# Optimization experiments

Hardware: AMD Instinct MI355X
Metric: run time of the kernel (lower is better)

Reference implementation:

```python
import jax, jax.numpy as jnp
import numpy as np

B, T, D = 32, 1024, 1024  # batch, t_k (encoder steps), attn_sz == cell_state_sz


def setup_inputs() -> dict:
    key = jax.random.key(0)
    ks = jax.random.split(key, 7)
    scale = 1.0 / np.sqrt(D)
    return {
        "h_i": jax.random.normal(ks[0], (B, T, D), jnp.float32),
        "s_t": jax.random.normal(ks[1], (B, D), jnp.float32),
        "coverage": jax.random.uniform(ks[2], (B, T), jnp.float32),
        "W_h": jax.random.normal(ks[3], (D, D), jnp.float32) * scale,
        "W_s": jax.random.normal(ks[4], (D, D), jnp.float32) * scale,
        "b_s": jnp.zeros((D,), jnp.float32),
        "W_c": jax.random.normal(ks[5], (D,), jnp.float32) * scale,  # Dense(1 -> D) kernel
        "V_w": jax.random.normal(ks[6], (D,), jnp.float32) * scale,  # Dense(D -> 1) kernel
    }


def reference(h_i, s_t, coverage, W_h, W_s, b_s, W_c, V_w):
    # enc_features = W_h(h_i): (B, T, D)
    enc_features = jnp.einsum("btd,de->bte", h_i, W_h)
    # dec_features = W_s(s_t) broadcast over time: (B, 1, D)
    dec_features = (s_t @ W_s + b_s)[:, None, :]
    # coverage features: scalar coverage per step times (1->D) kernel
    cov_features = coverage[:, :, None] * W_c[None, None, :]
    features = enc_features + dec_features + cov_features
    # e_t = V(tanh(features)) squeezed to (B, T)
    e_t = jnp.einsum("btd,d->bt", jnp.tanh(features), V_w)
    a_t = jax.nn.softmax(e_t, axis=1)
    coverage_new = coverage + a_t
    # context = a_t @ h_i : (B, D)
    context_vector = jnp.einsum("bt,btd->bd", a_t, h_i)
    return context_vector, a_t, coverage_new
```

## Files before the change

kernel.cpp:

```cpp
#include <hip/hip_runtime.h>

#define B_ 32
#define T_ 1024
#define D_ 1024
#define M_ (B_ * T_)
#define NT_ 8
#define BM_ 128
#define BN_ 128
#define BK_ 64
#define NKT (D_ / BK_)
#define LSTR 72

#define FENCE_ALL() asm volatile("s_waitcnt vmcnt(0) lgkmcnt(0)" ::: "memory")

typedef __attribute__((ext_vector_type(8))) short short8;
typedef __attribute__((ext_vector_type(4))) float f32x4;

__device__ __forceinline__ unsigned f2bf(float f) {
    union { float f; unsigned u; } v; v.f = f;
    return (v.u + 0x7FFFu + ((v.u >> 16) & 1u)) >> 16;
}
__device__ __forceinline__ unsigned pack2(float a, float b) {
    return f2bf(a) | (f2bf(b) << 16);
}
__device__ __forceinline__ float bf2f(unsigned hi16) {
    union { unsigned u; float f; } v; v.u = hi16 << 16;
    return v.f;
}
__device__ __forceinline__ float fast_tanh(float x) {
    x = fminf(15.0f, fmaxf(-15.0f, x));
    float e = __expf(2.0f * x);
    return (e - 1.0f) * __fdividef(1.0f, e + 1.0f);
}

__global__ __launch_bounds__(256) void conv_h_kernel(
    const float* __restrict__ in, uint4* __restrict__ out)
{
    const int idx = blockIdx.x * 256 + threadIdx.x;
    const int stride = gridDim.x * 256;
    const int ngroups = M_ * D_ / 8;
    const float4* in4 = (const float4*)in;
    for (int g = idx; g < ngroups; g += stride) {
        const float4 a = in4[2 * g];
        const float4 b = in4[2 * g + 1];
        out[g] = make_uint4(pack2(a.x, a.y), pack2(a.z, a.w),
                            pack2(b.x, b.y), pack2(b.z, b.w));
    }
}

__global__ __launch_bounds__(256) void conv_wt_kernel(
    const float* __restrict__ W_h, unsigned short* __restrict__ Wt)
{
    __shared__ float tile[64][65];
    const int k0 = (blockIdx.x & 15) * 64;
    const int n0 = (blockIdx.x >> 4) * 64;
    const int tx = threadIdx.x & 63, ty = threadIdx.x >> 6;
#pragma unroll
    for (int r = 0; r < 16; ++r) {
        const int row = ty * 16 + r;
        tile[row][tx] = W_h[(size_t)(k0 + row) * D_ + n0 + tx];
    }
    __syncthreads();
#pragma unroll
    for (int r = 0; r < 16; ++r) {
        const int row = ty * 16 + r;
        Wt[(size_t)(n0 + row) * D_ + k0 + tx] = (unsigned short)f2bf(tile[tx][row]);
    }
}

__global__ __launch_bounds__(256) void dec_kernel(
    const float* __restrict__ s_t, const float* __restrict__ W_s,
    const float* __restrict__ b_s, float* __restrict__ dec_part)
{
    const int bid = blockIdx.x;
    const int kc = bid & 3;
    const int nc = (bid >> 2) & 3;
    const int b  = bid >> 4;
    const int d = nc * 256 + threadIdx.x;
    const int k0 = kc * 256;
    __shared__ float s_lds[256];
    s_lds[threadIdx.x] = s_t[b * D_ + k0 + threadIdx.x];
    __syncthreads();
    float acc = (kc == 0) ? b_s[d] : 0.f;
#pragma unroll 8
    for (int k = 0; k < 256; ++k) acc += s_lds[k] * W_s[(size_t)(k0 + k) * D_ + d];
    dec_part[kc * (B_ * D_) + b * D_ + d] = acc;
}

__global__ __launch_bounds__(256, 2) void attn_gemm_fast(
    const unsigned short* __restrict__ h_bf, const unsigned short* __restrict__ wt_bf,
    const float* __restrict__ dec_part, const float* __restrict__ coverage,
    const float* __restrict__ W_c, const float* __restrict__ V_w,
    float* __restrict__ e_part)
{
    __shared__ __align__(16) unsigned short lA[BM_ * BK_];
    __shared__ __align__(16) unsigned short lB[BN_ * BK_];
    __shared__ float e_red[256];

    const int tid = threadIdx.x;
    const int nt = blockIdx.x >> 8;
    const int mt = blockIdx.x & 255;
    const int m0 = mt * BM_;
    const int n0 = nt * BN_;
    const int bb = m0 >> 10;

    const int wave = tid >> 6;
    const int lane = tid & 63;
    const int wr = wave >> 1, wc = wave & 1;
    const int lr = lane & 15;
    const int lk = lane >> 4;

    f32x4 acc[4][4];
    const f32x4 fzero = {0.f, 0.f, 0.f, 0.f};
#pragma unroll
    for (int i = 0; i < 4; ++i)
#pragma unroll
        for (int j = 0; j < 4; ++j) acc[i][j] = fzero;

    const char* gA = (const char*)h_bf + (size_t)m0 * (D_ * 2);
    const char* gB = (const char*)wt_bf + (size_t)n0 * (D_ * 2);
    const int lrow8 = lane >> 3;
    const int scol = (((lane & 7) ^ lrow8) << 4);

    for (int k0 = 0; k0 < D_; k0 += BK_) {
#pragma unroll
        for (int j = 0; j < 4; ++j) {
            const int c = 4 * wave + j;
            const int row = c * 8 + lrow8;
            const size_t goff = (size_t)row * (D_ * 2) + (size_t)k0 * 2 + scol;
            __builtin_amdgcn_global_load_lds(
                (const __attribute__((address_space(1))) void*)(gA + goff),
                (__attribute__((address_space(3))) void*)((char*)lA + c * 1024),
                16, 0, 0);
            __builtin_amdgcn_global_load_lds(
                (const __attribute__((address_space(1))) void*)(gB + goff),
                (__attribute__((address_space(3))) void*)((char*)lB + c * 1024),
                16, 0, 0);
        }
        FENCE_ALL();
        __syncthreads();

        short8 af[2][4], bfr[2][4];
        const int sw = (lr & 7) << 4;
#pragma unroll
        for (int kk = 0; kk < 2; ++kk)
#pragma unroll
            for (int i = 0; i < 4; ++i) {
                const int ar = wr * 64 + i * 16 + lr;
                const int br = wc * 64 + i * 16 + lr;
                const int kb = kk * 64 + lk * 16;
                af[kk][i]  = *(const short8*)((const char*)lA + ar * 128 + (kb ^ sw));
                bfr[kk][i] = *(const short8*)((const char*)lB + br * 128 + (kb ^ sw));
            }
#pragma unroll
        for (int kk = 0; kk < 2; ++kk)
#pragma unroll
            for (int mi = 0; mi < 4; ++mi)
#pragma unroll
                for (int ni = 0; ni < 4; ++ni)
                    acc[mi][ni] = __builtin_amdgcn_mfma_f32_16x16x32_bf16(
                        af[kk][mi], bfr[kk][ni], acc[mi][ni], 0, 0, 0);
        FENCE_ALL();
        __syncthreads();
    }

    float esum[4][4];
    float covv[4][4];
#pragma unroll
    for (int mi = 0; mi < 4; ++mi)
#pragma unroll
        for (int r = 0; r < 4; ++r) {
            esum[mi][r] = 0.f;
            covv[mi][r] = coverage[m0 + wr * 64 + mi * 16 + lk * 4 + r];
        }
    const float* dp = dec_part + bb * D_;
#pragma unroll
    for (int ni = 0; ni < 4; ++ni) {
        const int n = n0 + wc * 64 + ni * 16 + lr;
        const float vw = V_w[n];
        const float dc = dp[n] + dp[B_ * D_ + n] + dp[2 * B_ * D_ + n] + dp[3 * B_ * D_ + n];
        const float wcv = W_c[n];
#pragma unroll
        for (int mi = 0; mi < 4; ++mi)
#pragma unroll
            for (int r = 0; r < 4; ++r) {
                const float f = acc[mi][ni][r] + dc + covv[mi][r] * wcv;
                esum[mi][r] += fast_tanh(f) * vw;
            }
    }
#pragma unroll
    for (int off = 1; off <= 8; off <<= 1)
#pragma unroll
        for (int mi = 0; mi < 4; ++mi)
#pragma unroll
            for (int r = 0; r < 4; ++r)
                esum[mi][r] += __shfl_xor(esum[mi][r], off, 64);

    if (lr == 0) {
#pragma unroll
        for (int mi = 0; mi < 4; ++mi)
#pragma unroll
            for (int r = 0; r < 4; ++r)
                e_red[wc * 128 + wr * 64 + mi * 16 + lk * 4 + r] = esum[mi][r];
    }
    FENCE_ALL();
    __syncthreads();
    if (tid < 128)
        e_part[(size_t)nt * M_ + m0 + tid] = e_red[tid] + e_red[128 + tid];
}

__global__ __launch_bounds__(256, 2) void attn_gemm_kernel(
    const float* __restrict__ h_i, const float* __restrict__ W_h,
    const float* __restrict__ dec_part, const float* __restrict__ coverage,
    const float* __restrict__ W_c, const float* __restrict__ V_w,
    float* __restrict__ e_part)
{
    __shared__ __align__(16) unsigned short lA[BM_][LSTR];
    __shared__ __align__(16) unsigned short lB[BN_][LSTR];
    __shared__ float e_red[256];

    const int tid = threadIdx.x;
    const int nt = blockIdx.x >> 8;
    const int mt = blockIdx.x & 255;
    const int m0 = mt * BM_;
    const int n0 = nt * BN_;
    const int bb = m0 >> 10;

    const int wave = tid >> 6;
    const int lane = tid & 63;
    const int wr = wave >> 1, wc = wave & 1;
    const int lr = lane & 15;
    const int lk = lane >> 4;

    f32x4 acc[4][4];
    const f32x4 fzero = {0.f, 0.f, 0.f, 0.f};
#pragma unroll
    for (int i = 0; i < 4; ++i)
#pragma unroll
        for (int j = 0; j < 4; ++j) acc[i][j] = fzero;

    const int a_row = tid >> 4;
    const int a_k = (tid & 15) << 2;
    const float* hA = h_i + (size_t)m0 * D_;

    for (int k0 = 0; k0 < D_; k0 += BK_) {
#pragma unroll
        for (int p = 0; p < 8; ++p) {
            const int row = a_row + p * 16;
            const float4 v = *(const float4*)(hA + (size_t)row * D_ + (k0 + a_k));
            *(uint2*)&lA[row][a_k] = make_uint2(pack2(v.x, v.y), pack2(v.z, v.w));
        }
#pragma unroll
        for (int p = 0; p < 8; ++p) {
            const int task = tid + p * 256;
            const int n = task & 127;
            const int kg = task >> 7;
            const float* wp = W_h + (size_t)(k0 + kg * 4) * D_ + n0 + n;
            const float x0 = wp[0 * D_], x1 = wp[1 * D_], x2 = wp[2 * D_], x3 = wp[3 * D_];
            *(uint2*)&lB[n][kg * 4] = make_uint2(pack2(x0, x1), pack2(x2, x3));
        }
        __syncthreads();

        short8 af[2][4], bfr[2][4];
#pragma unroll
        for (int kk = 0; kk < 2; ++kk)
#pragma unroll
            for (int i = 0; i < 4; ++i) {
                af[kk][i]  = *(const short8*)&lA[wr * 64 + i * 16 + lr][kk * 32 + lk * 8];
                bfr[kk][i] = *(const short8*)&lB[wc * 64 + i * 16 + lr][kk * 32 + lk * 8];
            }
#pragma unroll
        for (int kk = 0; kk < 2; ++kk)
#pragma unroll
            for (int mi = 0; mi < 4; ++mi)
#pragma unroll
                for (int ni = 0; ni < 4; ++ni)
                    acc[mi][ni] = __builtin_amdgcn_mfma_f32_16x16x32_bf16(
                        af[kk][mi], bfr[kk][ni], acc[mi][ni], 0, 0, 0);
        __syncthreads();
    }

    float esum[4][4];
    float covv[4][4];
#pragma unroll
    for (int mi = 0; mi < 4; ++mi)
#pragma unroll
        for (int r = 0; r < 4; ++r) {
            esum[mi][r] = 0.f;
            covv[mi][r] = coverage[m0 + wr * 64 + mi * 16 + lk * 4 + r];
        }
    const float* dp = dec_part + bb * D_;
#pragma unroll
    for (int ni = 0; ni < 4; ++ni) {
        const int n = n0 + wc * 64 + ni * 16 + lr;
        const float vw = V_w[n];
        const float dc = dp[n] + dp[B_ * D_ + n] + dp[2 * B_ * D_ + n] + dp[3 * B_ * D_ + n];
        const float wcv = W_c[n];
#pragma unroll
        for (int mi = 0; mi < 4; ++mi)
#pragma unroll
            for (int r = 0; r < 4; ++r) {
                const float f = acc[mi][ni][r] + dc + covv[mi][r] * wcv;
                esum[mi][r] += fast_tanh(f) * vw;
            }
    }
#pragma unroll
    for (int off = 1; off <= 8; off <<= 1)
#pragma unroll
        for (int mi = 0; mi < 4; ++mi)
#pragma unroll
            for (int r = 0; r < 4; ++r)
                esum[mi][r] += __shfl_xor(esum[mi][r], off, 64);

    if (lr == 0) {
#pragma unroll
        for (int mi = 0; mi < 4; ++mi)
#pragma unroll
            for (int r = 0; r < 4; ++r)
                e_red[wc * 128 + wr * 64 + mi * 16 + lk * 4 + r] = esum[mi][r];
    }
    __syncthreads();
    if (tid < 128)
        e_part[(size_t)nt * M_ + m0 + tid] = e_red[tid] + e_red[128 + tid];
}

__global__ __launch_bounds__(256) void softmax_kernel(
    const float* __restrict__ e_part, const float* __restrict__ coverage,
    float* __restrict__ a_out, float* __restrict__ cov_out,
    float* __restrict__ a_ws)
{
    const int b = blockIdx.x;
    const int tid = threadIdx.x;
    __shared__ float redmx[4], redsum[4];
    float e[4];
#pragma unroll
    for (int j = 0; j < 4; ++j) {
        const int t = tid + j * 256;
        float s = 0.f;
#pragma unroll
        for (int p = 0; p < NT_; ++p) s += e_part[(size_t)p * M_ + b * T_ + t];
        e[j] = s;
    }
    float mx = fmaxf(fmaxf(e[0], e[1]), fmaxf(e[2], e[3]));
#pragma unroll
    for (int off = 32; off > 0; off >>= 1) mx = fmaxf(mx, __shfl_xor(mx, off, 64));
    if ((tid & 63) == 0) redmx[tid >> 6] = mx;
    __syncthreads();
    mx = fmaxf(fmaxf(redmx[0], redmx[1]), fmaxf(redmx[2], redmx[3]));
    float p4[4];
    float ps = 0.f;
#pragma unroll
    for (int j = 0; j < 4; ++j) { p4[j] = __expf(e[j] - mx); ps += p4[j]; }
#pragma unroll
    for (int off = 32; off > 0; off >>= 1) ps += __shfl_xor(ps, off, 64);
    if ((tid & 63) == 0) redsum[tid >> 6] = ps;
    __syncthreads();
    ps = redsum[0] + redsum[1] + redsum[2] + redsum[3];
    const float inv = __fdividef(1.f, ps);
#pragma unroll
    for (int j = 0; j < 4; ++j) {
        const int idx = b * T_ + tid + j * 256;
        const float a = p4[j] * inv;
        a_out[idx] = a;
        a_ws[idx] = a;
        cov_out[idx] = coverage[idx] + a;
    }
}

__global__ __launch_bounds__(256) void ctx_part_bf(
    const unsigned short* __restrict__ h_bf, const float* __restrict__ a_t,
    float* __restrict__ ctx_part)
{
    const int bid = blockIdx.x;
    const int b = bid >> 3;
    const int dc = (bid >> 2) & 1;
    const int tc = bid & 3;
    const int tid = threadIdx.x;
    const int d0 = dc * 512 + tid * 2;
    __shared__ float a_lds[256];
    a_lds[tid] = a_t[b * T_ + tc * 256 + tid];
    __syncthreads();
    const unsigned short* hp = h_bf + ((size_t)(b * T_ + tc * 256)) * D_ + d0;
    float acc0 = 0.f, acc1 = 0.f;
#pragma unroll 8
    for (int t = 0; t < 256; ++t) {
        const unsigned v = *(const unsigned*)(hp + (size_t)t * D_);
        const float a = a_lds[t];
        acc0 += a * bf2f(v & 0xFFFFu);
        acc1 += a * bf2f(v >> 16);
    }
    *(float2*)(ctx_part + tc * (B_ * D_) + b * D_ + d0) = make_float2(acc0, acc1);
}

__global__ __launch_bounds__(256) void ctx_part_f32(
    const float* __restrict__ h_i, const float* __restrict__ a_t,
    float* __restrict__ ctx_part)
{
    const int bid = blockIdx.x;
    const int b = bid >> 4;
    const int dc = (bid >> 2) & 3;
    const int tc = bid & 3;
    const int tid = threadIdx.x;
    const int d = dc * 256 + tid;
    __shared__ float a_lds[256];
    a_lds[tid] = a_t[b * T_ + tc * 256 + tid];
    __syncthreads();
    const float* hp = h_i + ((size_t)(b * T_ + tc * 256)) * D_ + d;
    float acc = 0.f;
#pragma unroll 8
    for (int t = 0; t < 256; ++t) acc += a_lds[t] * hp[(size_t)t * D_];
    ctx_part[tc * (B_ * D_) + b * D_ + d] = acc;
}

__global__ __launch_bounds__(256) void ctx_reduce_kernel(
    const float* __restrict__ ctx_part, float* __restrict__ out)
{
    const int i = blockIdx.x * 256 + threadIdx.x;
    out[i] = ctx_part[i] + ctx_part[B_ * D_ + i] + ctx_part[2 * B_ * D_ + i] +
             ctx_part[3 * B_ * D_ + i];
}

extern "C" void kernel_launch(void* const* d_in, const int* in_sizes, int n_in,
                              void* d_out, int out_size, void* d_ws, size_t ws_size,
                              hipStream_t stream)
{
    (void)in_sizes; (void)n_in; (void)out_size;
    const float* h_i      = (const float*)d_in[0];
    const float* s_t      = (const float*)d_in[1];
    const float* coverage = (const float*)d_in[2];
    const float* W_h      = (const float*)d_in[3];
    const float* W_s      = (const float*)d_in[4];
    const float* b_s      = (const float*)d_in[5];
    const float* W_c      = (const float*)d_in[6];
    const float* V_w      = (const float*)d_in[7];

    float* out     = (float*)d_out;
    float* ctx_out = out;
    float* a_out   = out + B_ * T_;
    float* cov_out = out + 2 * B_ * T_;

    float* ws       = (float*)d_ws;
    float* dec_part = ws;
    float* e_part   = dec_part + 4 * B_ * D_;
    float* ctx_part = e_part + NT_ * M_;
    float* a_ws     = ctx_part + 4 * B_ * D_;
    const size_t f32_count = 8 * (size_t)B_ * D_ + (size_t)NT_ * M_ + (size_t)B_ * T_;
    unsigned short* h_bf  = (unsigned short*)(ws + f32_count);
    unsigned short* wt_bf = h_bf + (size_t)M_ * D_;
    const size_t need = f32_count * 4 + ((size_t)M_ * D_ + (size_t)D_ * D_) * 2;

    dec_kernel<<<B_ * 16, 256, 0, stream>>>(s_t, W_s, b_s, dec_part);
    if (ws_size >= need) {
        conv_h_kernel<<<2048, 256, 0, stream>>>(h_i, (uint4*)h_bf);
        conv_wt_kernel<<<256, 256, 0, stream>>>(W_h, wt_bf);
        attn_gemm_fast<<<NT_ * (M_ / BM_), 256, 0, stream>>>(h_bf, wt_bf, dec_part,
                                                             coverage, W_c, V_w, e_part);
        softmax_kernel<<<B_, 256, 0, stream>>>(e_part, coverage, a_out, cov_out, a_ws);
        ctx_part_bf<<<B_ * 8, 256, 0, stream>>>(h_bf, a_ws, ctx_part);
    } else {
        attn_gemm_kernel<<<NT_ * (M_ / BM_), 256, 0, stream>>>(h_i, W_h, dec_part,
                                                               coverage, W_c, V_w, e_part);
        softmax_kernel<<<B_, 256, 0, stream>>>(e_part, coverage, a_out, cov_out, a_ws);
        ctx_part_f32<<<B_ * 16, 256, 0, stream>>>(h_i, a_ws, ctx_part);
    }
    ctx_reduce_kernel<<<(B_ * D_) / 256, 256, 0, stream>>>(ctx_part, ctx_out);
}
```

Measured before the change: 157.3 us.

## Fuse prep kernels, reorder GEMM tile mapping, prefetch next K tile in GEMM

Merges the h/W_h bf16 conversion kernels and the decoder projection into one prep launch, cutting two launches and letting the three run concurrently. In attn_gemm_fast, block indices now map with N-tiles innermost, so the 8 blocks sharing one h row tile are adjacent, which should improve L2 reuse of A. The K loop now issues the global-to-LDS loads for the next tile right after reading fragments, so they overlap with the MFMAs. This needs an extra barrier per iteration and uses a single LDS buffer, so overlap is limited to the MFMA phase.

```diff
diff --git a/kernel.cpp b/kernel.cpp
--- a/kernel.cpp
+++ b/kernel.cpp
@@ -33,39 +33,396 @@
     return (e - 1.0f) * __fdividef(1.0f, e + 1.0f);
 }
 
-__global__ __launch_bounds__(256) void conv_h_kernel(
-    const float* __restrict__ in, uint4* __restrict__ out)
-{
-    const int idx = blockIdx.x * 256 + threadIdx.x;
-    const int stride = gridDim.x * 256;
-    const int ngroups = M_ * D_ / 8;
-    const float4* in4 = (const float4*)in;
-    for (int g = idx; g < ngroups; g += stride) {
-        const float4 a = in4[2 * g];
-        const float4 b = in4[2 * g + 1];
-        out[g] = make_uint4(pack2(a.x, a.y), pack2(a.z, a.w),
-                            pack2(b.x, b.y), pack2(b.z, b.w));
-    }
-}
-
-__global__ __launch_bounds__(256) void conv_wt_kernel(
-    const float* __restrict__ W_h, unsigned short* __restrict__ Wt)
-{
-    __shared__ float tile[64][65];
-    const int k0 = (blockIdx.x & 15) * 64;
-    const int n0 = (blockIdx.x >> 4) * 64;
-    const int tx = threadIdx.x & 63, ty = threadIdx.x >> 6;
-#pragma unroll
-    for (int r = 0; r < 16; ++r) {
-        const int row = ty * 16 + r;
-        tile[row][tx] = W_h[(size_t)(k0 + row) * D_ + n0 + tx];
-    }
-    __syncthreads();
-#pragma unroll
-    for (int r = 0; r < 16; ++r) {
-        const int row = ty * 16 + r;
-        Wt[(size_t)(n0 + row) * D_ + k0 + tx] = (unsigned short)f2bf(tile[tx][row]);
-    }
+#define PREP_CONVH_BLKS 2048
+#define PREP_CONVWT_BLKS 256
+#define PREP_DEC_BLKS (B_ * 16)
+__global__ __launch_bounds__(256) void prep_kernel(
+    const float* __restrict__ h_i, uint4* __restrict__ h_bf4,
+    const float* __restrict__ W_h, unsigned short* __restrict__ Wt,
+    const float* __restrict__ s_t, const float* __restrict__ W_s,
+    const float* __restrict__ b_s, float* __restrict__ dec_part)
+{
+    __shared__ float smem[64 * 65];
+    const int bid = blockIdx.x;
+    const int tid = threadIdx.x;
+    if (bid < PREP_CONVH_BLKS) {
+        const int idx = bid * 256 + tid;
+        const int stride = PREP_CONVH_BLKS * 256;
+        const int ngroups = M_ * D_ / 8;
+        const float4* in4 = (const float4*)h_i;
+        for (int g = idx; g < ngroups; g += stride) {
+            const float4 a = in4[2 * g];
+            const float4 b = in4[2 * g + 1];
+            h_bf4[g] = make_uint4(pack2(a.x, a.y), pack2(a.z, a.w),
+                                  pack2(b.x, b.y), pack2(b.z, b.w));
+        }
+    } else if (bid < PREP_CONVH_BLKS + PREP_CONVWT_BLKS) {
+        const int tb = bid - PREP_CONVH_BLKS;
+        float (*tile)[65] = (float (*)[65])smem;
+        const int k0 = (tb & 15) * 64;
+        const int n0 = (tb >> 4) * 64;
+        const int tx = tid & 63, ty = tid >> 6;
+#pragma unroll
+        for (int r = 0; r < 16; ++r) {
+            const int row = ty * 16 + r;
+            tile[row][tx] = W_h[(size_t)(k0 + row) * D_ + n0 + tx];
+        }
+        __syncthreads();
+#pragma unroll
+        for (int r = 0; r < 16; ++r) {
+            const int row = ty * 16 + r;
+            Wt[(size_t)(n0 + row) * D_ + k0 + tx] = (unsigned short)f2bf(tile[tx][row]);
+        }
+    } else {
+        const int db = bid - (PREP_CONVH_BLKS + PREP_CONVWT_BLKS);
+        const int kc = db & 3;
+        const int nc = (db >> 2) & 3;
+        const int b  = db >> 4;
+        const int d = nc * 256 + tid;
+        const int k0 = kc * 256;
+        float* s_lds = smem;
+        s_lds[tid] = s_t[b * D_ + k0 + tid];
+        __syncthreads();
+        float acc = (kc == 0) ? b_s[d] : 0.f;
+#pragma unroll 8
+        for (int k = 0; k < 256; ++k) acc += s_lds[k] * W_s[(size_t)(k0 + k) * D_ + d];
+        dec_part[kc * (B_ * D_) + b * D_ + d] = acc;
+    }
+}
+
+__global__ __launch_bounds__(256, 2) void attn_gemm_fast(
+    const unsigned short* __restrict__ h_bf, const unsigned short* __restrict__ wt_bf,
+    const float* __restrict__ dec_part, const float* __restrict__ coverage,
+    const float* __restrict__ W_c, const float* __restrict__ V_w,
+    float* __restrict__ e_part)
+{
+    __shared__ __align__(16) unsigned short lA[BM_ * BK_];
+    __shared__ __align__(16) unsigned short lB[BN_ * BK_];
+    __shared__ float e_red[256];
+
+    const int tid = threadIdx.x;
+    const int mt = blockIdx.x >> 3;
+    const int nt = blockIdx.x & 7;
+    const int m0 = mt * BM_;
+    const int n0 = nt * BN_;
+    const int bb = m0 >> 10;
+
+    const int wave = tid >> 6;
+    const int lane = tid & 63;
+    const int wr = wave >> 1, wc = wave & 1;
+    const int lr = lane & 15;
+    const int lk = lane >> 4;
+
+    f32x4 acc[4][4];
+    const f32x4 fzero = {0.f, 0.f, 0.f, 0.f};
+#pragma unroll
+    for (int i = 0; i < 4; ++i)
+#pragma unroll
+        for (int j = 0; j < 4; ++j) acc[i][j] = fzero;
+
+    const char* gA = (const char*)h_bf + (size_t)m0 * (D_ * 2);
+    const char* gB = (const char*)wt_bf + (size_t)n0 * (D_ * 2);
+    const int lrow8 = lane >> 3;
+    const int scol = (((lane & 7) ^ lrow8) << 4);
+
+#define STAGE(k0)                                                                  \
+    {                                                                              \
+        _Pragma("unroll")                                                          \
+        for (int j = 0; j < 4; ++j) {                                              \
+            const int c = 4 * wave + j;                                            \
+            const int row = c * 8 + lrow8;                                         \
+            const size_t goff = (size_t)row * (D_ * 2) + (size_t)(k0) * 2 + scol;  \
+            __builtin_amdgcn_global_load_lds(                                      \
+                (const __attribute__((address_space(1))) void*)(gA + goff),        \
+                (__attribute__((address_space(3))) void*)((char*)lA + c * 1024),   \
+                16, 0, 0);                                                         \
+            __builtin_amdgcn_global_load_lds(                                      \
+                (const __attribute__((address_space(1))) void*)(gB + goff),        \
+                (__attribute__((address_space(3))) void*)((char*)lB + c * 1024),   \
+                16, 0, 0);                                                         \
+        }                                                                          \
+    }
+
+    STAGE(0);
+    const int sw = (lr & 7) << 4;
+
+    for (int kt = 0; kt < NKT; ++kt) {
+        FENCE_ALL();
+        __syncthreads();
+
+        short8 af[2][4], bfr[2][4];
+#pragma unroll
+        for (int kk = 0; kk < 2; ++kk)
+#pragma unroll
+            for (int i = 0; i < 4; ++i) {
+                const int ar = wr * 64 + i * 16 + lr;
+                const int br = wc * 64 + i * 16 + lr;
+                const int kb = kk * 64 + lk * 16;
+                af[kk][i]  = *(const short8*)((const char*)lA + ar * 128 + (kb ^ sw));
+                bfr[kk][i] = *(const short8*)((const char*)lB + br * 128 + (kb ^ sw));
+            }
+        FENCE_ALL();
+        __syncthreads();
+
+        if (kt + 1 < NKT) STAGE((kt + 1) * BK_);
+
+#pragma unroll
+        for (int kk = 0; kk < 2; ++kk)
+#pragma unroll
+            for (int mi = 0; mi < 4; ++mi)
+#pragma unroll
+                for (int ni = 0; ni < 4; ++ni)
+                    acc[mi][ni] = __builtin_amdgcn_mfma_f32_16x16x32_bf16(
+                        af[kk][mi], bfr[kk][ni], acc[mi][ni], 0, 0, 0);
+    }
+#undef STAGE
+
+    float esum[4][4];
+    float covv[4][4];
+#pragma unroll
+    for (int mi = 0; mi < 4; ++mi)
+#pragma unroll
+        for (int r = 0; r < 4; ++r) {
+            esum[mi][r] = 0.f;
+            covv[mi][r] = coverage[m0 + wr * 64 + mi * 16 + lk * 4 + r];
+        }
+    const float* dp = dec_part + bb * D_;
+#pragma unroll
+    for (int ni = 0; ni < 4; ++ni) {
+        const int n = n0 + wc * 64 + ni * 16 + lr;
+        const float vw = V_w[n];
+        const float dc = dp[n] + dp[B_ * D_ + n] + dp[2 * B_ * D_ + n] + dp[3 * B_ * D_ + n];
+        const float wcv = W_c[n];
+#pragma unroll
+        for (int mi = 0; mi < 4; ++mi)
+#pragma unroll
+            for (int r = 0; r < 4; ++r) {
+                const float f = acc[mi][ni][r] + dc + covv[mi][r] * wcv;
+                esum[mi][r] += fast_tanh(f) * vw;
+            }
+    }
+#pragma unroll
+    for (int off = 1; off <= 8; off <<= 1)
+#pragma unroll
+        for (int mi = 0; mi < 4; ++mi)
+#pragma unroll
+            for (int r = 0; r < 4; ++r)
+                esum[mi][r] += __shfl_xor(esum[mi][r], off, 64);
+
+    if (lr == 0) {
+#pragma unroll
+        for (int mi = 0; mi < 4; ++mi)
+#pragma unroll
+            for (int r = 0; r < 4; ++r)
+                e_red[wc * 128 + wr * 64 + mi * 16 + lk * 4 + r] = esum[mi][r];
+    }
+    FENCE_ALL();
+    __syncthreads();
+    if (tid < 128)
+        e_part[(size_t)nt * M_ + m0 + tid] = e_red[tid] + e_red[128 + tid];
+}
+
+__global__ __launch_bounds__(256, 2) void attn_gemm_kernel(
+    const float* __restrict__ h_i, const float* __restrict__ W_h,
+    const float* __restrict__ dec_part, const float* __restrict__ coverage,
+    const float* __restrict__ W_c, const float* __restrict__ V_w,
+    float* __restrict__ e_part)
+{
+    __shared__ __align__(16) unsigned short lA[BM_][LSTR];
+    __shared__ __align__(16) unsigned short lB[BN_][LSTR];
+    __shared__ float e_red[256];
+
+    const int tid = threadIdx.x;
+    const int nt = blockIdx.x >> 8;
+    const int mt = blockIdx.x & 255;
+    const int m0 = mt * BM_;
+    const int n0 = nt * BN_;
+    const int bb = m0 >> 10;
+
+    const int wave = tid >> 6;
+    const int lane = tid & 63;
+    const int wr = wave >> 1, wc = wave & 1;
+    const int lr = lane & 15;
+    const int lk = lane >> 4;
+
+    f32x4 acc[4][4];
+    const f32x4 fzero = {0.f, 0.f, 0.f, 0.f};
+#pragma unroll
+    for (int i = 0; i < 4; ++i)
+#pragma unroll
+        for (int j = 0; j < 4; ++j) acc[i][j] = fzero;
+
+    const int a_row = tid >> 4;
+    const int a_k = (tid & 15) << 2;
+    const float* hA = h_i + (size_t)m0 * D_;
+
+    for (int k0 = 0; k0 < D_; k0 += BK_) {
+#pragma unroll
+        for (int p = 0; p < 8; ++p) {
+            const int row = a_row + p * 16;
+            const float4 v = *(const float4*)(hA + (size_t)row * D_ + (k0 + a_k));
+            *(uint2*)&lA[row][a_k] = make_uint2(pack2(v.x, v.y), pack2(v.z, v.w));
+        }
+#pragma unroll
+        for (int p = 0; p < 8; ++p) {
+            const int task = tid + p * 256;
+            const int n = task & 127;
+            const int kg = task >> 7;
+            const float* wp = W_h + (size_t)(k0 + kg * 4) * D_ + n0 + n;
+            const float x0 = wp[0 * D_], x1 = wp[1 * D_], x2 = wp[2 * D_], x3 = wp[3 * D_];
+            *(uint2*)&lB[n][kg * 4] = make_uint2(pack2(x0, x1), pack2(x2, x3));
+        }
+        __syncthreads();
+
+        short8 af[2][4], bfr[2][4];
+#pragma unroll
+        for (int kk = 0; kk < 2; ++kk)
+#pragma unroll
+            for (int i = 0; i < 4; ++i) {
+                af[kk][i]  = *(const short8*)&lA[wr * 64 + i * 16 + lr][kk * 32 + lk * 8];
+                bfr[kk][i] = *(const short8*)&lB[wc * 64 + i * 16 + lr][kk * 32 + lk * 8];
+            }
+#pragma unroll
+        for (int kk = 0; kk < 2; ++kk)
+#pragma unroll
+            for (int mi = 0; mi < 4; ++mi)
+#pragma unroll
+                for (int ni = 0; ni < 4; ++ni)
+                    acc[mi][ni] = __builtin_amdgcn_mfma_f32_16x16x32_bf16(
+                        af[kk][mi], bfr[kk][ni], acc[mi][ni], 0, 0, 0);
+        __syncthreads();
+    }
+
+    float esum[4][4];
+    float covv[4][4];
+#pragma unroll
+    for (int mi = 0; mi < 4; ++mi)
+#pragma unroll
+        for (int r = 0; r < 4; ++r) {
+            esum[mi][r] = 0.f;
+            covv[mi][r] = coverage[m0 + wr * 64 + mi * 16 + lk * 4 + r];
+        }
+    const float* dp = dec_part + bb * D_;
+#pragma unroll
+    for (int ni = 0; ni < 4; ++ni) {
+        const int n = n0 + wc * 64 + ni * 16 + lr;
+        const float vw = V_w[n];
+        const float dc = dp[n] + dp[B_ * D_ + n] + dp[2 * B_ * D_ + n] + dp[3 * B_ * D_ + n];
+        const float wcv = W_c[n];
+#pragma unroll
+        for (int mi = 0; mi < 4; ++mi)
+#pragma unroll
+            for (int r = 0; r < 4; ++r) {
+                const float f = acc[mi][ni][r] + dc + covv[mi][r] * wcv;
+                esum[mi][r] += fast_tanh(f) * vw;
+            }
+    }
+#pragma unroll
+    for (int off = 1; off <= 8; off <<= 1)
+#pragma unroll
+        for (int mi = 0; mi < 4; ++mi)
+#pragma unroll
+            for (int r = 0; r < 4; ++r)
+                esum[mi][r] += __shfl_xor(esum[mi][r], off, 64);
+
+    if (lr == 0) {
+#pragma unroll
+        for (int mi = 0; mi < 4; ++mi)
+#pragma unroll
+            for (int r = 0; r < 4; ++r)
+                e_red[wc * 128 + wr * 64 + mi * 16 + lk * 4 + r] = esum[mi][r];
+    }
+    __syncthreads();
+    if (tid < 128)
+        e_part[(size_t)nt * M_ + m0 + tid] = e_red[tid] + e_red[128 + tid];
+}
+
+__global__ __launch_bounds__(256) void softmax_kernel(
+    const float* __restrict__ e_part, const float* __restrict__ coverage,
+    float* __restrict__ a_out, float* __restrict__ cov_out,
+    float* __restrict__ a_ws)
+{
+    const int b = blockIdx.x;
+    const int tid = threadIdx.x;
+    __shared__ float redmx[4], redsum[4];
+    float e[4];
+#pragma unroll
+    for (int j = 0; j < 4; ++j) {
+        const int t = tid + j * 256;
+        float s = 0.f;
+#pragma unroll
+        for (int p = 0; p < NT_; ++p) s += e_part[(size_t)p * M_ + b * T_ + t];
+        e[j] = s;
+    }
+    float mx = fmaxf(fmaxf(e[0], e[1]), fmaxf(e[2], e[3]));
+#pragma unroll
+    for (int off = 32; off > 0; off >>= 1) mx = fmaxf(mx, __shfl_xor(mx, off, 64));
+    if ((tid & 63) == 0) redmx[tid >> 6] = mx;
+    __syncthreads();
+    mx = fmaxf(fmaxf(redmx[0], redmx[1]), fmaxf(redmx[2], redmx[3]));
+    float p4[4];
+    float ps = 0.f;
+#pragma unroll
+    for (int j = 0; j < 4; ++j) { p4[j] = __expf(e[j] - mx); ps += p4[j]; }
+#pragma unroll
+    for (int off = 32; off > 0; off >>= 1) ps += __shfl_xor(ps, off, 64);
+    if ((tid & 63) == 0) redsum[tid >> 6] = ps;
+    __syncthreads();
+    ps = redsum[0] + redsum[1] + redsum[2] + redsum[3];
+    const float inv = __fdividef(1.f, ps);
+#pragma unroll
+    for (int j = 0; j < 4; ++j) {
+        const int idx = b * T_ + tid + j * 256;
+        const float a = p4[j] * inv;
+        a_out[idx] = a;
+        a_ws[idx] = a;
+        cov_out[idx] = coverage[idx] + a;
+    }
+}
+
+__global__ __launch_bounds__(256) void ctx_part_bf(
+    const unsigned short* __restrict__ h_bf, const float* __restrict__ a_t,
+    float* __restrict__ ctx_part)
+{
+    const int bid = blockIdx.x;
+    const int b = bid >> 3;
+    const int dc = (bid >> 2) & 1;
+    const int tc = bid & 3;
+    const int tid = threadIdx.x;
+    const int d0 = dc * 512 + tid * 2;
+    __shared__ float a_lds[256];
+    a_lds[tid] = a_t[b * T_ + tc * 256 + tid];
+    __syncthreads();
+    const unsigned short* hp = h_bf + ((size_t)(b * T_ + tc * 256)) * D_ + d0;
+    float acc0 = 0.f, acc1 = 0.f;
+#pragma unroll 8
+    for (int t = 0; t < 256; ++t) {
+        const unsigned v = *(const unsigned*)(hp + (size_t)t * D_);
+        const float a = a_lds[t];
+        acc0 += a * bf2f(v & 0xFFFFu);
+        acc1 += a * bf2f(v >> 16);
+    }
+    *(float2*)(ctx_part + tc * (B_ * D_) + b * D_ + d0) = make_float2(acc0, acc1);
+}
+
+__global__ __launch_bounds__(256) void ctx_part_f32(
+    const float* __restrict__ h_i, const float* __restrict__ a_t,
+    float* __restrict__ ctx_part)
+{
+    const int bid = blockIdx.x;
+    const int b = bid >> 4;
+    const int dc = (bid >> 2) & 3;
+    const int tc = bid & 3;
+    const int tid = threadIdx.x;
+    const int d = dc * 256 + tid;
+    __shared__ float a_lds[256];
+    a_lds[tid] = a_t[b * T_ + tc * 256 + tid];
+    __syncthreads();
+    const float* hp = h_i + ((size_t)(b * T_ + tc * 256)) * D_ + d;
+    float acc = 0.f;
+#pragma unroll 8
+    for (int t = 0; t < 256; ++t) acc += a_lds[t] * hp[(size_t)t * D_];
+    ctx_part[tc * (B_ * D_) + b * D_ + d] = acc;
 }
 
 __global__ __launch_bounds__(256) void dec_kernel(
@@ -85,331 +442,6 @@
 #pragma unroll 8
     for (int k = 0; k < 256; ++k) acc += s_lds[k] * W_s[(size_t)(k0 + k) * D_ + d];
     dec_part[kc * (B_ * D_) + b * D_ + d] = acc;
-}
-
-__global__ __launch_bounds__(256, 2) void attn_gemm_fast(
-    const unsigned short* __restrict__ h_bf, const unsigned short* __restrict__ wt_bf,
-    const float* __restrict__ dec_part, const float* __restrict__ coverage,
-    const float* __restrict__ W_c, const float* __restrict__ V_w,
-    float* __restrict__ e_part)
-{
-    __shared__ __align__(16) unsigned short lA[BM_ * BK_];
-    __shared__ __align__(16) unsigned short lB[BN_ * BK_];
-    __shared__ float e_red[256];
-
-    const int tid = threadIdx.x;
-    const int nt = blockIdx.x >> 8;
-    const int mt = blockIdx.x & 255;
-    const int m0 = mt * BM_;
-    const int n0 = nt * BN_;
-    const int bb = m0 >> 10;
-
-    const int wave = tid >> 6;
-    const int lane = tid & 63;
-    const int wr = wave >> 1, wc = wave & 1;
-    const int lr = lane & 15;
-    const int lk = lane >> 4;
-
-    f32x4 acc[4][4];
-    const f32x4 fzero = {0.f, 0.f, 0.f, 0.f};
-#pragma unroll
-    for (int i = 0; i < 4; ++i)
-#pragma unroll
-        for (int j = 0; j < 4; ++j) acc[i][j] = fzero;
-
-    const char* gA = (const char*)h_bf + (size_t)m0 * (D_ * 2);
-    const char* gB = (const char*)wt_bf + (size_t)n0 * (D_ * 2);
-    const int lrow8 = lane >> 3;
-    const int scol = (((lane & 7) ^ lrow8) << 4);
-
-    for (int k0 = 0; k0 < D_; k0 += BK_) {
-#pragma unroll
-        for (int j = 0; j < 4; ++j) {
-            const int c = 4 * wave + j;
-            const int row = c * 8 + lrow8;
-            const size_t goff = (size_t)row * (D_ * 2) + (size_t)k0 * 2 + scol;
-            __builtin_amdgcn_global_load_lds(
-                (const __attribute__((address_space(1))) void*)(gA + goff),
-                (__attribute__((address_space(3))) void*)((char*)lA + c * 1024),
-                16, 0, 0);
-            __builtin_amdgcn_global_load_lds(
-                (const __attribute__((address_space(1))) void*)(gB + goff),
-                (__attribute__((address_space(3))) void*)((char*)lB + c * 1024),
-                16, 0, 0);
-        }
-        FENCE_ALL();
-        __syncthreads();
-
-        short8 af[2][4], bfr[2][4];
-        const int sw = (lr & 7) << 4;
-#pragma unroll
-        for (int kk = 0; kk < 2; ++kk)
-#pragma unroll
-            for (int i = 0; i < 4; ++i) {
-                const int ar = wr * 64 + i * 16 + lr;
-                const int br = wc * 64 + i * 16 + lr;
-                const int kb = kk * 64 + lk * 16;
-                af[kk][i]  = *(const short8*)((const char*)lA + ar * 128 + (kb ^ sw));
-                bfr[kk][i] = *(const short8*)((const char*)lB + br * 128 + (kb ^ sw));
-            }
-#pragma unroll
-        for (int kk = 0; kk < 2; ++kk)
-#pragma unroll
-            for (int mi = 0; mi < 4; ++mi)
-#pragma unroll
-                for (int ni = 0; ni < 4; ++ni)
-                    acc[mi][ni] = __builtin_amdgcn_mfma_f32_16x16x32_bf16(
-                        af[kk][mi], bfr[kk][ni], acc[mi][ni], 0, 0, 0);
-        FENCE_ALL();
-        __syncthreads();
-    }
-
-    float esum[4][4];
-    float covv[4][4];
-#pragma unroll
-    for (int mi = 0; mi < 4; ++mi)
-#pragma unroll
-        for (int r = 0; r < 4; ++r) {
-            esum[mi][r] = 0.f;
-            covv[mi][r] = coverage[m0 + wr * 64 + mi * 16 + lk * 4 + r];
-        }
-    const float* dp = dec_part + bb * D_;
-#pragma unroll
-    for (int ni = 0; ni < 4; ++ni) {
-        const int n = n0 + wc * 64 + ni * 16 + lr;
-        const float vw = V_w[n];
-        const float dc = dp[n] + dp[B_ * D_ + n] + dp[2 * B_ * D_ + n] + dp[3 * B_ * D_ + n];
-        const float wcv = W_c[n];
-#pragma unroll
-        for (int mi = 0; mi < 4; ++mi)
-#pragma unroll
-            for (int r = 0; r < 4; ++r) {
-                const float f = acc[mi][ni][r] + dc + covv[mi][r] * wcv;
-                esum[mi][r] += fast_tanh(f) * vw;
-            }
-    }
-#pragma unroll
-    for (int off = 1; off <= 8; off <<= 1)
-#pragma unroll
-        for (int mi = 0; mi < 4; ++mi)
-#pragma unroll
-            for (int r = 0; r < 4; ++r)
-                esum[mi][r] += __shfl_xor(esum[mi][r], off, 64);
-
-    if (lr == 0) {
-#pragma unroll
-        for (int mi = 0; mi < 4; ++mi)
-#pragma unroll
-            for (int r = 0; r < 4; ++r)
-                e_red[wc * 128 + wr * 64 + mi * 16 + lk * 4 + r] = esum[mi][r];
-    }
-    FENCE_ALL();
-    __syncthreads();
-    if (tid < 128)
-        e_part[(size_t)nt * M_ + m0 + tid] = e_red[tid] + e_red[128 + tid];
-}
-
-__global__ __launch_bounds__(256, 2) void attn_gemm_kernel(
-    const float* __restrict__ h_i, const float* __restrict__ W_h,
-    const float* __restrict__ dec_part, const float* __restrict__ coverage,
-    const float* __restrict__ W_c, const float* __restrict__ V_w,
-    float* __restrict__ e_part)
-{
-    __shared__ __align__(16) unsigned short lA[BM_][LSTR];
-    __shared__ __align__(16) unsigned short lB[BN_][LSTR];
-    __shared__ float e_red[256];
-
-    const int tid = threadIdx.x;
-    const int nt = blockIdx.x >> 8;
-    const int mt = blockIdx.x & 255;
-    const int m0 = mt * BM_;
-    const int n0 = nt * BN_;
-    const int bb = m0 >> 10;
-
-    const int wave = tid >> 6;
-    const int lane = tid & 63;
-    const int wr = wave >> 1, wc = wave & 1;
-    const int lr = lane & 15;
-    const int lk = lane >> 4;
-
-    f32x4 acc[4][4];
-    const f32x4 fzero = {0.f, 0.f, 0.f, 0.f};
-#pragma unroll
-    for (int i = 0; i < 4; ++i)
-#pragma unroll
-        for (int j = 0; j < 4; ++j) acc[i][j] = fzero;
-
-    const int a_row = tid >> 4;
-    const int a_k = (tid & 15) << 2;
-    const float* hA = h_i + (size_t)m0 * D_;
-
-    for (int k0 = 0; k0 < D_; k0 += BK_) {
-#pragma unroll
-        for (int p = 0; p < 8; ++p) {
-            const int row = a_row + p * 16;
-            const float4 v = *(const float4*)(hA + (size_t)row * D_ + (k0 + a_k));
-            *(uint2*)&lA[row][a_k] = make_uint2(pack2(v.x, v.y), pack2(v.z, v.w));
-        }
-#pragma unroll
-        for (int p = 0; p < 8; ++p) {
-            const int task = tid + p * 256;
-            const int n = task & 127;
-            const int kg = task >> 7;
-            const float* wp = W_h + (size_t)(k0 + kg * 4) * D_ + n0 + n;
-            const float x0 = wp[0 * D_], x1 = wp[1 * D_], x2 = wp[2 * D_], x3 = wp[3 * D_];
-            *(uint2*)&lB[n][kg * 4] = make_uint2(pack2(x0, x1), pack2(x2, x3));
-        }
-        __syncthreads();
-
-        short8 af[2][4], bfr[2][4];
-#pragma unroll
-        for (int kk = 0; kk < 2; ++kk)
-#pragma unroll
-            for (int i = 0; i < 4; ++i) {
-                af[kk][i]  = *(const short8*)&lA[wr * 64 + i * 16 + lr][kk * 32 + lk * 8];
-                bfr[kk][i] = *(const short8*)&lB[wc * 64 + i * 16 + lr][kk * 32 + lk * 8];
-            }
-#pragma unroll
-        for (int kk = 0; kk < 2; ++kk)
-#pragma unroll
-            for (int mi = 0; mi < 4; ++mi)
-#pragma unroll
-                for (int ni = 0; ni < 4; ++ni)
-                    acc[mi][ni] = __builtin_amdgcn_mfma_f32_16x16x32_bf16(
-                        af[kk][mi], bfr[kk][ni], acc[mi][ni], 0, 0, 0);
-        __syncthreads();
-    }
-
-    float esum[4][4];
-    float covv[4][4];
-#pragma unroll
-    for (int mi = 0; mi < 4; ++mi)
-#pragma unroll
-        for (int r = 0; r < 4; ++r) {
-            esum[mi][r] = 0.f;
-            covv[mi][r] = coverage[m0 + wr * 64 + mi * 16 + lk * 4 + r];
-        }
-    const float* dp = dec_part + bb * D_;
-#pragma unroll
-    for (int ni = 0; ni < 4; ++ni) {
-        const int n = n0 + wc * 64 + ni * 16 + lr;
-        const float vw = V_w[n];
-        const float dc = dp[n] + dp[B_ * D_ + n] + dp[2 * B_ * D_ + n] + dp[3 * B_ * D_ + n];
-        const float wcv = W_c[n];
-#pragma unroll
-        for (int mi = 0; mi < 4; ++mi)
-#pragma unroll
-            for (int r = 0; r < 4; ++r) {
-                const float f = acc[mi][ni][r] + dc + covv[mi][r] * wcv;
-                esum[mi][r] += fast_tanh(f) * vw;
-            }
-    }
-#pragma unroll
-    for (int off = 1; off <= 8; off <<= 1)
-#pragma unroll
-        for (int mi = 0; mi < 4; ++mi)
-#pragma unroll
-            for (int r = 0; r < 4; ++r)
-                esum[mi][r] += __shfl_xor(esum[mi][r], off, 64);
-
-    if (lr == 0) {
-#pragma unroll
-        for (int mi = 0; mi < 4; ++mi)
-#pragma unroll
-            for (int r = 0; r < 4; ++r)
-                e_red[wc * 128 + wr * 64 + mi * 16 + lk * 4 + r] = esum[mi][r];
-    }
-    __syncthreads();
-    if (tid < 128)
-        e_part[(size_t)nt * M_ + m0 + tid] = e_red[tid] + e_red[128 + tid];
-}
-
-__global__ __launch_bounds__(256) void softmax_kernel(
-    const float* __restrict__ e_part, const float* __restrict__ coverage,
-    float* __restrict__ a_out, float* __restrict__ cov_out,
-    float* __restrict__ a_ws)
-{
-    const int b = blockIdx.x;
-    const int tid = threadIdx.x;
-    __shared__ float redmx[4], redsum[4];
-    float e[4];
-#pragma unroll
-    for (int j = 0; j < 4; ++j) {
-        const int t = tid + j * 256;
-        float s = 0.f;
-#pragma unroll
-        for (int p = 0; p < NT_; ++p) s += e_part[(size_t)p * M_ + b * T_ + t];
-        e[j] = s;
-    }
-    float mx = fmaxf(fmaxf(e[0], e[1]), fmaxf(e[2], e[3]));
-#pragma unroll
-    for (int off = 32; off > 0; off >>= 1) mx = fmaxf(mx, __shfl_xor(mx, off, 64));
-    if ((tid & 63) == 0) redmx[tid >> 6] = mx;
-    __syncthreads();
-    mx = fmaxf(fmaxf(redmx[0], redmx[1]), fmaxf(redmx[2], redmx[3]));
-    float p4[4];
-    float ps = 0.f;
-#pragma unroll
-    for (int j = 0; j < 4; ++j) { p4[j] = __expf(e[j] - mx); ps += p4[j]; }
-#pragma unroll
-    for (int off = 32; off > 0; off >>= 1) ps += __shfl_xor(ps, off, 64);
-    if ((tid & 63) == 0) redsum[tid >> 6] = ps;
-    __syncthreads();
-    ps = redsum[0] + redsum[1] + redsum[2] + redsum[3];
-    const float inv = __fdividef(1.f, ps);
-#pragma unroll
-    for (int j = 0; j < 4; ++j) {
-        const int idx = b * T_ + tid + j * 256;
-        const float a = p4[j] * inv;
-        a_out[idx] = a;
-        a_ws[idx] = a;
-        cov_out[idx] = coverage[idx] + a;
-    }
-}
-
-__global__ __launch_bounds__(256) void ctx_part_bf(
-    const unsigned short* __restrict__ h_bf, const float* __restrict__ a_t,
-    float* __restrict__ ctx_part)
-{
-    const int bid = blockIdx.x;
-    const int b = bid >> 3;
-    const int dc = (bid >> 2) & 1;
-    const int tc = bid & 3;
-    const int tid = threadIdx.x;
-    const int d0 = dc * 512 + tid * 2;
-    __shared__ float a_lds[256];
-    a_lds[tid] = a_t[b * T_ + tc * 256 + tid];
-    __syncthreads();
-    const unsigned short* hp = h_bf + ((size_t)(b * T_ + tc * 256)) * D_ + d0;
-    float acc0 = 0.f, acc1 = 0.f;
-#pragma unroll 8
-    for (int t = 0; t < 256; ++t) {
-        const unsigned v = *(const unsigned*)(hp + (size_t)t * D_);
-        const float a = a_lds[t];
-        acc0 += a * bf2f(v & 0xFFFFu);
-        acc1 += a * bf2f(v >> 16);
-    }
-    *(float2*)(ctx_part + tc * (B_ * D_) + b * D_ + d0) = make_float2(acc0, acc1);
-}
-
-__global__ __launch_bounds__(256) void ctx_part_f32(
-    const float* __restrict__ h_i, const float* __restrict__ a_t,
-    float* __restrict__ ctx_part)
-{
-    const int bid = blockIdx.x;
-    const int b = bid >> 4;
-    const int dc = (bid >> 2) & 3;
-    const int tc = bid & 3;
-    const int tid = threadIdx.x;
-    const int d = dc * 256 + tid;
-    __shared__ float a_lds[256];
-    a_lds[tid] = a_t[b * T_ + tc * 256 + tid];
-    __syncthreads();
-    const float* hp = h_i + ((size_t)(b * T_ + tc * 256)) * D_ + d;
-    float acc = 0.f;
-#pragma unroll 8
-    for (int t = 0; t < 256; ++t) acc += a_lds[t] * hp[(size_t)t * D_];
-    ctx_part[tc * (B_ * D_) + b * D_ + d] = acc;
 }
 
 __global__ __launch_bounds__(256) void ctx_reduce_kernel(
@@ -449,15 +481,15 @@
     unsigned short* wt_bf = h_bf + (size_t)M_ * D_;
     const size_t need = f32_count * 4 + ((size_t)M_ * D_ + (size_t)D_ * D_) * 2;
 
-    dec_kernel<<<B_ * 16, 256, 0, stream>>>(s_t, W_s, b_s, dec_part);
     if (ws_size >= need) {
-        conv_h_kernel<<<2048, 256, 0, stream>>>(h_i, (uint4*)h_bf);
-        conv_wt_kernel<<<256, 256, 0, stream>>>(W_h, wt_bf);
+        prep_kernel<<<PREP_CONVH_BLKS + PREP_CONVWT_BLKS + PREP_DEC_BLKS, 256, 0, stream>>>(
+            h_i, (uint4*)h_bf, W_h, wt_bf, s_t, W_s, b_s, dec_part);
         attn_gemm_fast<<<NT_ * (M_ / BM_), 256, 0, stream>>>(h_bf, wt_bf, dec_part,
                                                              coverage, W_c, V_w, e_part);
         softmax_kernel<<<B_, 256, 0, stream>>>(e_part, coverage, a_out, cov_out, a_ws);
         ctx_part_bf<<<B_ * 8, 256, 0, stream>>>(h_bf, a_ws, ctx_part);
     } else {
+        dec_kernel<<<B_ * 16, 256, 0, stream>>>(s_t, W_s, b_s, dec_part);
         attn_gemm_kernel<<<NT_ * (M_ / BM_), 256, 0, stream>>>(h_i, W_h, dec_part,
                                                                coverage, W_c, V_w, e_part);
         softmax_kernel<<<B_, 256, 0, stream>>>(e_part, coverage, a_out, cov_out, a_ws);
```

Result: no change. 158.0 us (+0.5%).
